# Kernel optimization log

Measured on AMD Instinct MI355X. Metric: run time of the kernel, lower is better.

## Reference

```python
import jax, jax.numpy as jnp
import numpy as np

H = W = 9
C = 16
D = 34
NHEAD = 2
HDIM = D // NHEAD  # 17
FF = 2048
NLAYERS = 2
EPS = 1e-5


def setup_inputs() -> dict:
    key = jax.random.key(0)
    ks = jax.random.split(key, 16)
    s = 0.05
    return {
        "obs": jax.random.normal(ks[0], (2, H, W), dtype=jnp.float32),
        "conv1_w": jax.random.normal(ks[1], (16, 2, 3, 3), dtype=jnp.float32) * s,
        "conv1_b": jnp.zeros((16,), jnp.float32),
        "conv2_w": jax.random.normal(ks[2], (16, 16, 3, 3), dtype=jnp.float32) * s,
        "conv2_b": jnp.zeros((16,), jnp.float32),
        "in_proj_w": jax.random.normal(ks[3], (NLAYERS, 3 * D, D), dtype=jnp.float32) * s,
        "in_proj_b": jnp.zeros((NLAYERS, 3 * D), jnp.float32),
        "out_proj_w": jax.random.normal(ks[4], (NLAYERS, D, D), dtype=jnp.float32) * s,
        "out_proj_b": jnp.zeros((NLAYERS, D), jnp.float32),
        "lin1_w": jax.random.normal(ks[5], (NLAYERS, FF, D), dtype=jnp.float32) * s,
        "lin1_b": jnp.zeros((NLAYERS, FF), jnp.float32),
        "lin2_w": jax.random.normal(ks[6], (NLAYERS, D, FF), dtype=jnp.float32) * s,
        "lin2_b": jnp.zeros((NLAYERS, D), jnp.float32),
        "ln1_g": jnp.ones((NLAYERS, D), jnp.float32),
        "ln1_b": jnp.zeros((NLAYERS, D), jnp.float32),
        "ln2_g": jnp.ones((NLAYERS, D), jnp.float32),
        "ln2_b": jnp.zeros((NLAYERS, D), jnp.float32),
    }


def _layer_norm(x, g, b):
    m = jnp.mean(x, axis=-1, keepdims=True)
    v = jnp.mean(jnp.square(x - m), axis=-1, keepdims=True)
    return (x - m) * jax.lax.rsqrt(v + EPS) * g + b


def _encoder_layer(x, ipw, ipb, opw, opb, l1w, l1b, l2w, l2b, g1, b1, g2, b2):
    # x: [S, D]. Post-norm TransformerEncoderLayer, eval mode (no dropout).
    S = x.shape[0]
    qkv = x @ ipw.T + ipb  # [S, 3D]
    q, k, v = jnp.split(qkv, 3, axis=-1)
    q = q.reshape(S, NHEAD, HDIM).transpose(1, 0, 2)  # [h, S, d]
    k = k.reshape(S, NHEAD, HDIM).transpose(1, 0, 2)
    v = v.reshape(S, NHEAD, HDIM).transpose(1, 0, 2)
    scores = jnp.einsum("hqd,hkd->hqk", q, k) / jnp.sqrt(jnp.float32(HDIM))
    attn = jax.nn.softmax(scores, axis=-1)
    o = jnp.einsum("hqk,hkd->hqd", attn, v)  # [h, S, d]
    o = o.transpose(1, 0, 2).reshape(S, D)
    o = o @ opw.T + opb
    x = _layer_norm(x + o, g1, b1)
    f = jax.nn.relu(x @ l1w.T + l1b) @ l2w.T + l2b
    return _layer_norm(x + f, g2, b2)


def _conv(x, w, b):
    y = jax.lax.conv_general_dilated(
        x, w, window_strides=(1, 1), padding="SAME",
        dimension_numbers=("NCHW", "OIHW", "NCHW"))
    return jax.nn.relu(y + b[None, :, None, None])


def reference(obs, conv1_w, conv1_b, conv2_w, conv2_b, in_proj_w, in_proj_b,
              out_proj_w, out_proj_b, lin1_w, lin1_b, lin2_w, lin2_b,
              ln1_g, ln1_b, ln2_g, ln2_b):
    x = obs[None]  # [1, 2, H, W]
    x = _conv(x, conv1_w, conv1_b)
    x = _conv(x, conv2_w, conv2_b)
    hw = H * W
    cell_emb = x[0].reshape(C, hw).T  # [hw, C]
    idx = jnp.arange(hw)
    r = (idx // W).astype(jnp.float32)
    c = (idx % W).astype(jnp.float32)
    dx = (r[:, None] - r[None, :]) / ((H - 1) / 2.0)  # [hw, hw]
    dy = (c[:, None] - c[None, :]) / ((W - 1) / 2.0)
    tok_i = jnp.broadcast_to(cell_emb[:, None, :], (hw, hw, C))
    tok_j = jnp.broadcast_to(cell_emb[None, :, :], (hw, hw, C))
    rel = jnp.stack([dx, dy], axis=-1)  # [hw, hw, 2]
    tokens = jnp.concatenate([tok_i, tok_j, rel], axis=-1).reshape(hw * hw, D)
    for l in range(NLAYERS):
        tokens = _encoder_layer(
            tokens, in_proj_w[l], in_proj_b[l], out_proj_w[l], out_proj_b[l],
            lin1_w[l], lin1_b[l], lin2_w[l], lin2_b[l],
            ln1_g[l], ln1_b[l], ln2_g[l], ln2_b[l])
    agent_idx = jnp.argmax(obs[0].reshape(-1))
    start = agent_idx * hw
    agent_tokens = jax.lax.dynamic_slice(tokens, (start, 0), (hw, D))
    return agent_tokens.mean(axis=0)  # [D]
```

## Files before the change

### kernel.cpp

```cpp
#include <hip/hip_runtime.h>
#include <hip/hip_bf16.h>

#define HH 9
#define WW 9
#define HW 81
#define CC 16
#define DD 34
#define SS 6561
#define NHEAD 2
#define HD 17
#define FF 2048
#define EPSF 1e-5f

#define NTILES 52
#define NSPLIT2 26
#define QB 64

#define NIP 7168
#define NOP 3072
#define NW1 131072
#define NW2 98304
#define NLTOT (NIP + NOP + NW1 + NW2)
#define LPREP_BLOCKS 1872
#define NKF 425984
#define NVF 212992
#define NV16 13312
#define ZERO_WORDS 332800
#define ZERO_BLOCKS 1300

#define NEAB 124416
#define NVFL1 12288
#define KSPLIT 8

typedef __attribute__((ext_vector_type(8))) short bf16x8;
typedef __attribute__((ext_vector_type(4))) float f32x4;

__device__ __forceinline__ unsigned short f2b(float f) {
  unsigned int u = __float_as_uint(f);
  u += 0x7fffu + ((u >> 16) & 1u);
  return (unsigned short)(u >> 16);
}

__global__ __launch_bounds__(256) void prep_kernel(
    const float* __restrict__ obs, const float* __restrict__ w1, const float* __restrict__ b1,
    const float* __restrict__ w2, const float* __restrict__ b2,
    float* __restrict__ cell, int* __restrict__ aidx,
    const float* __restrict__ ipw, const float* __restrict__ opw,
    const float* __restrict__ l1w, const float* __restrict__ l2w,
    unsigned short* __restrict__ ipwp, unsigned short* __restrict__ opwp,
    unsigned short* __restrict__ w1p, unsigned short* __restrict__ w2p,
    unsigned short* __restrict__ kfp, unsigned short* __restrict__ vfp,
    float* __restrict__ v16) {
  int bx = blockIdx.x;
  int t = threadIdx.x;
  if (bx == 0) {
    __shared__ float s_obs[2][11][11];
    __shared__ float s_w1[288];
    __shared__ float s_w2[2304];
    __shared__ float s_b1[16], s_b2[16];
    __shared__ float y1[CC][121];
    for (int i = t; i < 2 * 121; i += 256) ((float*)s_obs)[i] = 0.f;
    for (int i = t; i < CC * 121; i += 256) ((float*)y1)[i] = 0.f;
    for (int i = t; i < 288; i += 256) s_w1[i] = w1[i];
    for (int i = t; i < 2304; i += 256) s_w2[i] = w2[i];
    if (t < 16) { s_b1[t] = b1[t]; s_b2[t] = b2[t]; }
    __syncthreads();
    for (int i = t; i < 2 * HW; i += 256) {
      int ic = i / HW, p = i % HW;
      s_obs[ic][1 + p / WW][1 + p % WW] = obs[i];
    }
    __syncthreads();
    if (t == 0) {
      int best = 0; float bv = s_obs[0][1][1];
      for (int p = 1; p < HW; p++) {
        float v = s_obs[0][1 + p / WW][1 + p % WW];
        if (v > bv) { bv = v; best = p; }
      }
      *aidx = best;
    }
    for (int idx = t; idx < CC * HW; idx += 256) {
      int c = idx / HW, p = idx % HW;
      int i = p / WW, j = p % WW;
      float acc = s_b1[c];
#pragma unroll
      for (int ic = 0; ic < 2; ic++)
#pragma unroll
        for (int di = 0; di < 3; di++)
#pragma unroll
          for (int dj = 0; dj < 3; dj++)
            acc += s_obs[ic][i + di][j + dj] * s_w1[((c * 2 + ic) * 3 + di) * 3 + dj];
      y1[c][(i + 1) * 11 + (j + 1)] = fmaxf(acc, 0.f);
    }
    __syncthreads();
    for (int idx = t; idx < CC * HW; idx += 256) {
      int c = idx / HW, p = idx % HW;
      int i = p / WW, j = p % WW;
      float acc = s_b2[c];
#pragma unroll
      for (int ic = 0; ic < CC; ic++)
#pragma unroll
        for (int di = 0; di < 3; di++)
#pragma unroll
          for (int dj = 0; dj < 3; dj++)
            acc += y1[ic][(i + di) * 11 + (j + dj)] * s_w2[((c * CC + ic) * 3 + di) * 3 + dj];
      cell[p * CC + c] = fmaxf(acc, 0.f);
    }
  } else if (bx <= LPREP_BLOCKS) {
    int i = (bx - 1) * 256 + t;
    int layer = i / NLTOT;
    int r = i % NLTOT;
    if (r < NIP) {
      int n = r >> 6, k = r & 63;
      ipwp[layer * NIP + r] =
          (n < 102 && k < DD) ? f2b(ipw[(size_t)layer * 102 * DD + n * DD + k]) : (unsigned short)0;
    } else if (r < NIP + NOP) {
      int rr = r - NIP;
      int n = rr >> 6, k = rr & 63;
      opwp[layer * NOP + rr] =
          (n < DD && k < DD) ? f2b(opw[(size_t)layer * DD * DD + n * DD + k]) : (unsigned short)0;
    } else if (r < NIP + NOP + NW1) {
      int rr = r - NIP - NOP;
      int f = rr >> 6, k = rr & 63;
      w1p[layer * NW1 + rr] =
          (k < DD) ? f2b(l1w[(size_t)layer * FF * DD + f * DD + k]) : (unsigned short)0;
    } else {
      int rr = r - NIP - NOP - NW1;
      int d = rr >> 11, kk = rr & 2047;
      w2p[layer * NW2 + rr] =
          (d < DD) ? f2b(l2w[(size_t)layer * DD * FF + d * FF + kk]) : (unsigned short)0;
    }
  } else {
    int zi = (bx - 1 - LPREP_BLOCKS) * 256 + t;
    if (zi < NKF / 2) ((unsigned int*)kfp)[zi] = 0u;
    else if (zi < NKF / 2 + NVF / 2) ((unsigned int*)vfp)[zi - NKF / 2] = 0u;
    else if (zi < ZERO_WORDS) v16[zi - NKF / 2 - NVF / 2] = 0.f;
  }
}

__global__ __launch_bounds__(256) void ptprep_kernel(
    const float* __restrict__ cell, const float* __restrict__ ipw,
    const float* __restrict__ ipb, float* __restrict__ Pt) {
  int idx = blockIdx.x * 256 + threadIdx.x;
  if (idx >= 2 * HW * 102) return;
  int part = idx / (HW * 102);
  int rem = idx % (HW * 102);
  int a = rem / 102, n = rem % 102;
  float ra = (float)(a / WW) * 0.25f, ca = (float)(a % WW) * 0.25f;
  float acc;
  if (part == 0) {
    acc = ipb[n] + ipw[n * DD + 32] * ra + ipw[n * DD + 33] * ca;
    for (int f = 0; f < CC; f++) acc += ipw[n * DD + f] * cell[a * CC + f];
  } else {
    acc = -(ipw[n * DD + 32] * ra + ipw[n * DD + 33] * ca);
    for (int f = 0; f < CC; f++) acc += ipw[n * DD + CC + f] * cell[a * CC + f];
  }
  Pt[idx] = acc;
}

__global__ __launch_bounds__(256) void expprep_kernel(
    const float* __restrict__ Pt, float* __restrict__ eAB,
    unsigned short* __restrict__ vfragL1) {
  int idx = blockIdx.x * 256 + threadIdx.x;
  const float scale = 0.24253562503633297f;
  if (idx < NEAB) {
    int a = idx % 96; int rest = idx / 96;
    int row = rest % 81; rest /= 81;
    int ab = rest & 1, p = (rest >> 1) & 1, h = rest >> 2;
    float e = 0.f;
    if (a < HW) {
      const float* qrow = Pt + (size_t)ab * (HW * 102) + row * 102 + h * HD;
      const float* krow = Pt + (size_t)p * (HW * 102) + a * 102 + DD + h * HD;
      float dot = 0.f;
#pragma unroll
      for (int d = 0; d < HD; d++) dot += qrow[d] * krow[d];
      e = __expf(fminf(dot * scale, 40.f));
    }
    eAB[idx] = e;
  } else if (idx < NEAB + NVFL1) {
    int j = idx - NEAB;
    int a = j % 96; int rest = j / 96;
    int n = rest % 32; rest /= 32;
    int p = rest & 1, h = rest >> 1;
    float v = 0.f;
    if (a < HW) {
      if (n < HD) v = Pt[(size_t)p * (HW * 102) + a * 102 + 2 * DD + h * HD + n];
      else if (n == HD) v = 1.f;
    }
    vfragL1[((size_t)(h * 2 + p) * 32 + n) * 96 + a] = f2b(v);
  }
}

__global__ __launch_bounds__(256) void fl1_kernel(
    const float* __restrict__ cell, const float* __restrict__ eAB,
    const unsigned short* __restrict__ vfragL1,
    const unsigned short* __restrict__ opwp, const float* __restrict__ opb,
    const float* __restrict__ g1v, const float* __restrict__ b1v,
    const unsigned short* __restrict__ w1p, const unsigned short* __restrict__ w2p,
    const float* __restrict__ fb1, const float* __restrict__ fb2,
    const float* __restrict__ g2v, const float* __restrict__ b2v,
    float* __restrict__ x) {
  __shared__ __align__(16) unsigned short sE[4][16 * 96];
  __shared__ __align__(16) unsigned short soA[16 * 72];
  __shared__ float sxF[16][35];
  __shared__ __align__(16) unsigned short sxA2[16 * 72];
  __shared__ float sxF2[16][35];
  __shared__ __align__(16) unsigned short hw_[4][16 * 40];
  __shared__ float yred[4][16][49];
  int t = threadIdx.x;
  int w = t >> 6, lane = t & 63, quad = lane >> 4, col = lane & 15;
  int r0 = blockIdx.x * 16;
  int nr = min(16, SS - r0);

  for (int i = t; i < 16 * 72; i += 256) { soA[i] = 0; sxA2[i] = 0; }
  for (int i = t; i < 16 * 35; i += 256) { ((float*)sxF)[i] = 0.f; ((float*)sxF2)[i] = 0.f; }
  for (int i = t; i < nr * DD; i += 256) {
    int r = i / DD, d = i - r * DD;
    int row = r0 + r;
    int ii = row / HW, jj = row - ii * HW;
    float v;
    if (d < CC) v = cell[ii * CC + d];
    else if (d < 2 * CC) v = cell[jj * CC + (d - CC)];
    else if (d == 32) v = (float)((ii / WW) - (jj / WW)) * 0.25f;
    else v = (float)((ii % WW) - (jj % WW)) * 0.25f;
    sxF[r][d] = v;
  }

  {
    int h = w >> 1, p = w & 1;
    const float* eA = eAB + ((size_t)((h * 2 + p) * 2 + 0) * 81) * 96;
    const float* eB = eAB + ((size_t)((h * 2 + p) * 2 + 1) * 81) * 96;
    int tl = lane >> 2, asub = lane & 3;
    int row = r0 + tl;
    int tc = row < SS ? row : SS - 1;
    int it = tc / HW, jt = tc - it * HW;
    const float* eAr = eA + it * 96 + asub * 24;
    const float* eBr = eB + jt * 96 + asub * 24;
    unsigned short etmp[24];
#pragma unroll
    for (int k = 0; k < 24; k++) etmp[k] = f2b(eAr[k] * eBr[k]);
    unsigned short* Eb = &sE[w][tl * 96 + asub * 24];
#pragma unroll
    for (int k = 0; k < 3; k++)
      *(bf16x8*)(Eb + k * 8) = *(bf16x8*)(etmp + k * 8);
    const unsigned short* vf = vfragL1 + (size_t)(h * 2 + p) * 32 * 96;
    f32x4 acc0 = {0.f, 0.f, 0.f, 0.f}, acc1 = {0.f, 0.f, 0.f, 0.f};
#pragma unroll
    for (int c = 0; c < 3; c++) {
      bf16x8 ea = *(const bf16x8*)&sE[w][col * 96 + c * 32 + quad * 8];
      bf16x8 vb0 = *(const bf16x8*)&vf[col * 96 + c * 32 + quad * 8];
      bf16x8 vb1 = *(const bf16x8*)&vf[(16 + col) * 96 + c * 32 + quad * 8];
      acc0 = __builtin_amdgcn_mfma_f32_16x16x32_bf16(ea, vb0, acc0, 0, 0, 0);
      acc1 = __builtin_amdgcn_mfma_f32_16x16x32_bf16(ea, vb1, acc1, 0, 0, 0);
    }
    float Sr[4];
#pragma unroll
    for (int r = 0; r < 4; r++) Sr[r] = __shfl(acc1[r], (lane & 48) + 1);
#pragma unroll
    for (int r = 0; r < 4; r++) {
      int rr = quad * 4 + r;
      float inv = 1.f / Sr[r];
      yred[w][rr][col] = acc0[r] * inv;
      if (col == 0) yred[w][rr][16] = acc1[r] * inv;
    }
  }
  __syncthreads();
  for (int i = t; i < 16 * DD; i += 256) {
    int r = i / DD, dd = i - r * DD;
    int h2 = dd / HD, d2 = dd - h2 * HD;
    soA[r * 72 + dd] = f2b(yred[2 * h2][r][d2] + yred[2 * h2 + 1][r][d2]);
  }
  __syncthreads();

  if (w == 0) {
    bf16x8 a0 = *(const bf16x8*)&soA[col * 72 + quad * 8];
    bf16x8 a1 = *(const bf16x8*)&soA[col * 72 + 32 + quad * 8];
    f32x4 y[3];
#pragma unroll
    for (int nt = 0; nt < 3; nt++) {
      int n = nt * 16 + col;
      bf16x8 b0 = *(const bf16x8*)&opwp[n * 64 + quad * 8];
      bf16x8 b1 = *(const bf16x8*)&opwp[n * 64 + 32 + quad * 8];
      f32x4 acc = {0.f, 0.f, 0.f, 0.f};
      acc = __builtin_amdgcn_mfma_f32_16x16x32_bf16(a0, b0, acc, 0, 0, 0);
      y[nt] = __builtin_amdgcn_mfma_f32_16x16x32_bf16(a1, b1, acc, 0, 0, 0);
    }
    float yv[3][4];
    float s1[4] = {0.f, 0.f, 0.f, 0.f}, s2[4] = {0.f, 0.f, 0.f, 0.f};
#pragma unroll
    for (int nt = 0; nt < 3; nt++) {
      int d = nt * 16 + col;
      bool vd = d < DD;
      float ob = vd ? opb[d] : 0.f;
#pragma unroll
      for (int r = 0; r < 4; r++) {
        int row = quad * 4 + r;
        float v = vd ? (y[nt][r] + ob + sxF[row][d]) : 0.f;
        yv[nt][r] = v;
        s1[r] += v;
        s2[r] += v * v;
      }
    }
#pragma unroll
    for (int msk = 1; msk <= 8; msk <<= 1)
#pragma unroll
      for (int r = 0; r < 4; r++) {
        s1[r] += __shfl_xor(s1[r], msk);
        s2[r] += __shfl_xor(s2[r], msk);
      }
#pragma unroll
    for (int r = 0; r < 4; r++) {
      int row = quad * 4 + r;
      float mean = s1[r] * (1.f / DD);
      float var = s2[r] * (1.f / DD) - mean * mean;
      float rs = rsqrtf(var + EPSF);
#pragma unroll
      for (int nt = 0; nt < 3; nt++) {
        int d = nt * 16 + col;
        if (d < DD) {
          float o = (yv[nt][r] - mean) * rs * g1v[d] + b1v[d];
          sxF2[row][d] = o;
          sxA2[row * 72 + d] = f2b(o);
        }
      }
    }
  }
  __syncthreads();

  bf16x8 a0 = *(const bf16x8*)&sxA2[col * 72 + quad * 8];
  bf16x8 a1 = *(const bf16x8*)&sxA2[col * 72 + 32 + quad * 8];
  unsigned short* myh = &hw_[w][0];
  f32x4 acc3[3];
#pragma unroll
  for (int nt = 0; nt < 3; nt++) acc3[nt] = (f32x4){0.f, 0.f, 0.f, 0.f};
  for (int kt = 0; kt < 16; kt++) {
    int fbase = kt * 128 + w * 32;
#pragma unroll
    for (int nt = 0; nt < 2; nt++) {
      int f = fbase + nt * 16 + col;
      bf16x8 b0f = *(const bf16x8*)&w1p[f * 64 + quad * 8];
      bf16x8 b1f = *(const bf16x8*)&w1p[f * 64 + 32 + quad * 8];
      f32x4 hacc = {0.f, 0.f, 0.f, 0.f};
      hacc = __builtin_amdgcn_mfma_f32_16x16x32_bf16(a0, b0f, hacc, 0, 0, 0);
      hacc = __builtin_amdgcn_mfma_f32_16x16x32_bf16(a1, b1f, hacc, 0, 0, 0);
      float bias = fb1[f];
#pragma unroll
      for (int r = 0; r < 4; r++) {
        float hv = fmaxf(hacc[r] + bias, 0.f);
        myh[(quad * 4 + r) * 40 + nt * 16 + col] = f2b(hv);
      }
    }
    bf16x8 pa = *(const bf16x8*)&myh[col * 40 + quad * 8];
#pragma unroll
    for (int nt = 0; nt < 3; nt++) {
      int n = nt * 16 + col;
      bf16x8 wb = *(const bf16x8*)&w2p[(size_t)n * FF + fbase + quad * 8];
      acc3[nt] = __builtin_amdgcn_mfma_f32_16x16x32_bf16(pa, wb, acc3[nt], 0, 0, 0);
    }
  }
#pragma unroll
  for (int nt = 0; nt < 3; nt++)
#pragma unroll
    for (int r = 0; r < 4; r++)
      yred[w][quad * 4 + r][nt * 16 + col] = acc3[nt][r];
  __syncthreads();
  if (w == 0) {
    float yv[3][4];
    float s1[4] = {0.f, 0.f, 0.f, 0.f}, s2[4] = {0.f, 0.f, 0.f, 0.f};
#pragma unroll
    for (int nt = 0; nt < 3; nt++) {
      int d = nt * 16 + col;
      bool valid = d < DD;
      float b2x = valid ? fb2[d] : 0.f;
#pragma unroll
      for (int r = 0; r < 4; r++) {
        int row = quad * 4 + r;
        float v = yred[0][row][nt * 16 + col] + yred[1][row][nt * 16 + col]
                + yred[2][row][nt * 16 + col] + yred[3][row][nt * 16 + col];
        v = valid ? (v + b2x + sxF2[row][d]) : 0.f;
        yv[nt][r] = v;
        s1[r] += v;
        s2[r] += v * v;
      }
    }
#pragma unroll
    for (int msk = 1; msk <= 8; msk <<= 1)
#pragma unroll
      for (int r = 0; r < 4; r++) {
        s1[r] += __shfl_xor(s1[r], msk);
        s2[r] += __shfl_xor(s2[r], msk);
      }
#pragma unroll
    for (int r = 0; r < 4; r++) {
      int row = quad * 4 + r;
      if (row >= nr) continue;
      float mean = s1[r] * (1.f / DD);
      float var = s2[r] * (1.f / DD) - mean * mean;
      float rs = rsqrtf(var + EPSF);
#pragma unroll
      for (int nt = 0; nt < 3; nt++) {
        int d = nt * 16 + col;
        if (d < DD)
          x[(size_t)(r0 + row) * DD + d] = (yv[nt][r] - mean) * rs * g2v[d] + b2v[d];
      }
    }
  }
}

__global__ __launch_bounds__(256) void qkv2_kernel(
    const float* __restrict__ x, const unsigned short* __restrict__ ipwp,
    const float* __restrict__ ipb, const int* __restrict__ abase,
    float* __restrict__ qkv, unsigned short* __restrict__ kfp,
    unsigned short* __restrict__ vfp, float* __restrict__ v16) {
  __shared__ __align__(16) unsigned short sxA[32 * 72];
  int t = threadIdx.x;
  int w = t >> 6, lane = t & 63, quad = lane >> 4, col = lane & 15;
  int m0 = (w & 1) * 16, half = w >> 1;
  bool qpart = blockIdx.x >= 206;
  int row0 = qpart ? (abase[0] * HW + (blockIdx.x - 206) * 32) : blockIdx.x * 32;
  int nr = min(32, SS - row0);
  for (int i = t; i < 32 * 72; i += 256) sxA[i] = 0;
  __syncthreads();
  for (int i = t; i < nr * DD; i += 256) {
    int r = i / DD, d = i - r * DD;
    sxA[r * 72 + d] = f2b(x[(size_t)(row0 + r) * DD + d]);
  }
  __syncthreads();
  bf16x8 a0 = *(const bf16x8*)&sxA[(m0 + col) * 72 + quad * 8];
  bf16x8 a1 = *(const bf16x8*)&sxA[(m0 + col) * 72 + 32 + quad * 8];
  if (!qpart) {
    int ntc = half ? 2 : 3;
    for (int nt2 = 0; nt2 < ntc; nt2++) {
      int nt = half * 3 + nt2;
      int n = DD + nt * 16 + col;
      int nc = n < 112 ? n : 111;
      bf16x8 b0 = *(const bf16x8*)&ipwp[nc * 64 + quad * 8];
      bf16x8 b1 = *(const bf16x8*)&ipwp[nc * 64 + 32 + quad * 8];
      f32x4 acc = {0.f, 0.f, 0.f, 0.f};
      acc = __builtin_amdgcn_mfma_f32_16x16x32_bf16(a0, b0, acc, 0, 0, 0);
      acc = __builtin_amdgcn_mfma_f32_16x16x32_bf16(a1, b1, acc, 0, 0, 0);
      if (n < 102) {
        float bias = ipb[n];
        int kd = n - DD;
#pragma unroll
        for (int r = 0; r < 4; r++) {
          int m = m0 + quad * 4 + r;
          if (m >= nr) continue;
          int tok = row0 + m;
          float val = acc[r] + bias;
          int T = tok >> 7, tl = tok & 127;
          if (kd < 2 * HD) {
            int h = kd >= HD;
            int d = kd - h * HD;
            int colf = tl >> 3, ntk = tl & 7;
            kfp[(((size_t)h * NTILES + T) * 8 + ntk) * 512 +
                ((d >> 3) * 16 + colf) * 8 + (d & 7)] = f2b(val);
          } else {
            int vd = kd - 2 * HD;
            int h = vd >= HD;
            int d = vd - h * HD;
            if (d < 16) {
              int c = tl >> 5, qf = (tl >> 3) & 3, j = tl & 7;
              vfp[(((size_t)h * NTILES + T) * 4 + c) * 512 +
                  (qf * 16 + d) * 8 + j] = f2b(val);
            } else {
              v16[(size_t)h * (NTILES * 128) + tok] = val;
            }
          }
        }
      }
    }
  } else {
    int ntc = half ? 1 : 2;
    for (int nt2 = 0; nt2 < ntc; nt2++) {
      int nt = half * 2 + nt2;
      int n = nt * 16 + col;
      bf16x8 b0 = *(const bf16x8*)&ipwp[n * 64 + quad * 8];
      bf16x8 b1 = *(const bf16x8*)&ipwp[n * 64 + 32 + quad * 8];
      f32x4 acc = {0.f, 0.f, 0.f, 0.f};
      acc = __builtin_amdgcn_mfma_f32_16x16x32_bf16(a0, b0, acc, 0, 0, 0);
      acc = __builtin_amdgcn_mfma_f32_16x16x32_bf16(a1, b1, acc, 0, 0, 0);
      if (n < DD) {
        float bias = ipb[n];
#pragma unroll
        for (int r = 0; r < 4; r++) {
          int m = row0 + m0 + quad * 4 + r;
          if (m < SS) qkv[(size_t)m * 102 + n] = acc[r] + bias;
        }
      }
    }
  }
}

__global__ __launch_bounds__(256) void attn2_kernel(
    const float* __restrict__ qkv, const unsigned short* __restrict__ kfp,
    const unsigned short* __restrict__ vfp, const float* __restrict__ v16,
    const int* __restrict__ abase,
    float* __restrict__ opart, float* __restrict__ lpart) {
  __shared__ __align__(16) unsigned short scb[4][16 * 136];
  int t = threadIdx.x, w = t >> 6, lane = t & 63, quad = lane >> 4, col = lane & 15;
  int h = blockIdx.y, sp = blockIdx.z;
  int base = abase[0] * HW;
  int q0 = blockIdx.x * QB;
  const float scale = 0.24253562503633297f;
  const unsigned short* kf = kfp + (size_t)h * (NTILES * 8 * 512);
  const unsigned short* vf = vfp + (size_t)h * (NTILES * 4 * 512);
  const float* v16h = v16 + (size_t)h * (NTILES * 128);
  unsigned short* myscb = &scb[w][0];

  int mq = base + q0 + w * 16 + col;
  int qc = mq < SS ? mq : SS - 1;
  bf16x8 aq;
#pragma unroll
  for (int j = 0; j < 8; j++) {
    int d = quad * 8 + j;
    aq[j] = (short)((d < HD) ? f2b(qkv[(size_t)qc * 102 + h * HD + d] * scale) : 0);
  }

  f32x4 oacc = {0.f, 0.f, 0.f, 0.f};
  float o16a[4] = {0.f, 0.f, 0.f, 0.f};
  float lreg[4] = {0.f, 0.f, 0.f, 0.f};

  for (int tile = sp; tile < NTILES; tile += NSPLIT2) {
    int k0 = tile * 128;
    const unsigned short* kt = kf + (size_t)tile * (8 * 512);
    f32x4 s[8];
#pragma unroll
    for (int nt = 0; nt < 8; nt++) {
      bf16x8 kb = *(const bf16x8*)(kt + nt * 512 + lane * 8);
      f32x4 z = {0.f, 0.f, 0.f, 0.f};
      s[nt] = __builtin_amdgcn_mfma_f32_16x16x32_bf16(aq, kb, z, 0, 0, 0);
    }
    if (k0 + 128 > SS) {
#pragma unroll
      for (int nt = 0; nt < 8; nt++)
        if (k0 + col * 8 + nt >= SS) {
          s[nt][0] = -1e30f; s[nt][1] = -1e30f; s[nt][2] = -1e30f; s[nt][3] = -1e30f;
        }
    }
#pragma unroll
    for (int r = 0; r < 4; r++) {
      bf16x8 pv;
      float psl = 0.f;
#pragma unroll
      for (int nt = 0; nt < 8; nt++) {
        float p = __expf(fminf(s[nt][r], 70.f));
        s[nt][r] = p;
        psl += p;
        pv[nt] = (short)f2b(p);
      }
      lreg[r] += psl;
      *(bf16x8*)(myscb + (quad * 4 + r) * 136 + col * 8) = pv;
    }
    f32x4 va = *(const f32x4*)(v16h + k0 + col * 8);
    f32x4 vb4 = *(const f32x4*)(v16h + k0 + col * 8 + 4);
#pragma unroll
    for (int r = 0; r < 4; r++) {
      o16a[r] += s[0][r] * va[0] + s[1][r] * va[1] + s[2][r] * va[2] + s[3][r] * va[3]
               + s[4][r] * vb4[0] + s[5][r] * vb4[1] + s[6][r] * vb4[2] + s[7][r] * vb4[3];
    }
    const unsigned short* vt = vf + (size_t)tile * (4 * 512);
#pragma unroll
    for (int c = 0; c < 4; c++) {
      bf16x8 pa = *(const bf16x8*)(myscb + col * 136 + c * 32 + quad * 8);
      bf16x8 vbf = *(const bf16x8*)(vt + c * 512 + lane * 8);
      oacc = __builtin_amdgcn_mfma_f32_16x16x32_bf16(pa, vbf, oacc, 0, 0, 0);
    }
  }
#pragma unroll
  for (int msk = 1; msk <= 8; msk <<= 1)
#pragma unroll
    for (int r = 0; r < 4; r++) {
      o16a[r] += __shfl_xor(o16a[r], msk);
      lreg[r] += __shfl_xor(lreg[r], msk);
    }
  size_t obase = ((size_t)sp * NHEAD + h) * 128;
#pragma unroll
  for (int r = 0; r < 4; r++) {
    int ql = q0 + w * 16 + quad * 4 + r;
    if (ql < HW) {
      opart[(obase + ql) * HD + col] = oacc[r];
      if (col == 0) {
        opart[(obase + ql) * HD + 16] = o16a[r];
        lpart[obase + ql] = lreg[r];
      }
    }
  }
}

__global__ __launch_bounds__(256) void fl2a_kernel(
    const float* __restrict__ opart, const float* __restrict__ lpart,
    const unsigned short* __restrict__ opwp, const float* __restrict__ opb,
    const float* __restrict__ g1v, const float* __restrict__ b1v,
    const unsigned short* __restrict__ w1p, const unsigned short* __restrict__ w2p,
    const float* __restrict__ fb1, const int* __restrict__ abase,
    const float* __restrict__ x, float* __restrict__ xln, float* __restrict__ ypart) {
  __shared__ __align__(16) unsigned short soA[16 * 72];
  __shared__ float sxF[16][35];
  __shared__ __align__(16) unsigned short sxA2[16 * 72];
  __shared__ float sxF2[16][35];
  __shared__ __align__(16) unsigned short hw_[4][16 * 40];
  __shared__ float yred[4][16][49];
  int t = threadIdx.x;
  int w = t >> 6, lane = t & 63, quad = lane >> 4, col = lane & 15;
  int sp = blockIdx.y;
  int base = abase[0] * HW;
  int ql0 = blockIdx.x * 16;
  int nr = min(16, HW - ql0);
  int r0 = base + ql0;

  for (int i = t; i < 16 * 72; i += 256) { soA[i] = 0; sxA2[i] = 0; }
  for (int i = t; i < 16 * 35; i += 256) { ((float*)sxF)[i] = 0.f; ((float*)sxF2)[i] = 0.f; }
  __syncthreads();
  for (int i = t; i < nr * DD; i += 256) {
    int r = i / DD, rem = i - r * DD;
    sxF[r][rem] = x[(size_t)(r0 + r) * DD + rem];
    int ql = ql0 + r;
    int h = rem / HD, d = rem - h * HD;
    float L = 0.f, O = 0.f;
#pragma unroll
    for (int s = 0; s < NSPLIT2; s++) {
      L += lpart[((size_t)s * NHEAD + h) * 128 + ql];
      O += opart[(((size_t)s * NHEAD + h) * 128 + ql) * HD + d];
    }
    soA[r * 72 + rem] = f2b(O / L);
  }
  __syncthreads();
  if (w == 0) {
    bf16x8 a0 = *(const bf16x8*)&soA[col * 72 + quad * 8];
    bf16x8 a1 = *(const bf16x8*)&soA[col * 72 + 32 + quad * 8];
    f32x4 y[3];
#pragma unroll
    for (int nt = 0; nt < 3; nt++) {
      int n = nt * 16 + col;
      bf16x8 b0 = *(const bf16x8*)&opwp[n * 64 + quad * 8];
      bf16x8 b1 = *(const bf16x8*)&opwp[n * 64 + 32 + quad * 8];
      f32x4 acc = {0.f, 0.f, 0.f, 0.f};
      acc = __builtin_amdgcn_mfma_f32_16x16x32_bf16(a0, b0, acc, 0, 0, 0);
      y[nt] = __builtin_amdgcn_mfma_f32_16x16x32_bf16(a1, b1, acc, 0, 0, 0);
    }
    float yv[3][4];
    float s1[4] = {0.f, 0.f, 0.f, 0.f}, s2[4] = {0.f, 0.f, 0.f, 0.f};
#pragma unroll
    for (int nt = 0; nt < 3; nt++) {
      int d = nt * 16 + col;
      bool vd = d < DD;
      float ob = vd ? opb[d] : 0.f;
#pragma unroll
      for (int r = 0; r < 4; r++) {
        int row = quad * 4 + r;
        float v = vd ? (y[nt][r] + ob + sxF[row][d]) : 0.f;
        yv[nt][r] = v;
        s1[r] += v;
        s2[r] += v * v;
      }
    }
#pragma unroll
    for (int msk = 1; msk <= 8; msk <<= 1)
#pragma unroll
      for (int r = 0; r < 4; r++) {
        s1[r] += __shfl_xor(s1[r], msk);
        s2[r] += __shfl_xor(s2[r], msk);
      }
#pragma unroll
    for (int r = 0; r < 4; r++) {
      int row = quad * 4 + r;
      float mean = s1[r] * (1.f / DD);
      float var = s2[r] * (1.f / DD) - mean * mean;
      float rs = rsqrtf(var + EPSF);
#pragma unroll
      for (int nt = 0; nt < 3; nt++) {
        int d = nt * 16 + col;
        if (d < DD) {
          float o = (yv[nt][r] - mean) * rs * g1v[d] + b1v[d];
          sxF2[row][d] = o;
          sxA2[row * 72 + d] = f2b(o);
          if (sp == 0 && row < nr)
            xln[(size_t)(ql0 + row) * DD + d] = o;
        }
      }
    }
  }
  __syncthreads();
  bf16x8 a0 = *(const bf16x8*)&sxA2[col * 72 + quad * 8];
  bf16x8 a1 = *(const bf16x8*)&sxA2[col * 72 + 32 + quad * 8];
  unsigned short* myh = &hw_[w][0];
  f32x4 acc3[3];
#pragma unroll
  for (int nt = 0; nt < 3; nt++) acc3[nt] = (f32x4){0.f, 0.f, 0.f, 0.f};
  for (int kt2 = 0; kt2 < 2; kt2++) {
    int kt = sp * 2 + kt2;
    int fbase = kt * 128 + w * 32;
#pragma unroll
    for (int nt = 0; nt < 2; nt++) {
      int f = fbase + nt * 16 + col;
      bf16x8 b0f = *(const bf16x8*)&w1p[f * 64 + quad * 8];
      bf16x8 b1f = *(const bf16x8*)&w1p[f * 64 + 32 + quad * 8];
      f32x4 hacc = {0.f, 0.f, 0.f, 0.f};
      hacc = __builtin_amdgcn_mfma_f32_16x16x32_bf16(a0, b0f, hacc, 0, 0, 0);
      hacc = __builtin_amdgcn_mfma_f32_16x16x32_bf16(a1, b1f, hacc, 0, 0, 0);
      float bias = fb1[f];
#pragma unroll
      for (int r = 0; r < 4; r++) {
        float hv = fmaxf(hacc[r] + bias, 0.f);
        myh[(quad * 4 + r) * 40 + nt * 16 + col] = f2b(hv);
      }
    }
    bf16x8 pa = *(const bf16x8*)&myh[col * 40 + quad * 8];
#pragma unroll
    for (int nt = 0; nt < 3; nt++) {
      int n = nt * 16 + col;
      bf16x8 wb = *(const bf16x8*)&w2p[(size_t)n * FF + fbase + quad * 8];
      acc3[nt] = __builtin_amdgcn_mfma_f32_16x16x32_bf16(pa, wb, acc3[nt], 0, 0, 0);
    }
  }
#pragma unroll
  for (int nt = 0; nt < 3; nt++)
#pragma unroll
    for (int r = 0; r < 4; r++)
      yred[w][quad * 4 + r][nt * 16 + col] = acc3[nt][r];
  __syncthreads();
  if (w == 0) {
    for (int i = lane; i < nr * DD; i += 64) {
      int r = i / DD, d = i - r * DD;
      float v = yred[0][r][d] + yred[1][r][d] + yred[2][r][d] + yred[3][r][d];
      ypart[((size_t)sp * HW + ql0 + r) * DD + d] = v;
    }
  }
}

__global__ __launch_bounds__(256) void fl2b_kernel(
    const float* __restrict__ ypart, const float* __restrict__ xln,
    const float* __restrict__ fb2, const float* __restrict__ g2v,
    const float* __restrict__ b2v, const int* __restrict__ abase,
    float* __restrict__ x) {
  int t = threadIdx.x;
  int row = blockIdx.x * 32 + (t >> 3);
  int s8 = t & 7;
  if (row >= HW) return;
  int base = abase[0] * HW;
  float yv[5];
  float s1 = 0.f, s2 = 0.f;
  int cnt = 0;
  for (int d = s8; d < DD; d += 8) {
    float v = fb2[d] + xln[(size_t)row * DD + d];
#pragma unroll
    for (int sp = 0; sp < KSPLIT; sp++)
      v += ypart[((size_t)sp * HW + row) * DD + d];
    yv[cnt++] = v;
    s1 += v;
    s2 += v * v;
  }
  s1 += __shfl_xor(s1, 1); s2 += __shfl_xor(s2, 1);
  s1 += __shfl_xor(s1, 2); s2 += __shfl_xor(s2, 2);
  s1 += __shfl_xor(s1, 4); s2 += __shfl_xor(s2, 4);
  float mean = s1 * (1.f / DD);
  float var = s2 * (1.f / DD) - mean * mean;
  float rs = rsqrtf(var + EPSF);
  cnt = 0;
  for (int d = s8; d < DD; d += 8)
    x[(size_t)(base + row) * DD + d] = (yv[cnt++] - mean) * rs * g2v[d] + b2v[d];
}

__global__ __launch_bounds__(64) void final_kernel(
    const float* __restrict__ x, const int* __restrict__ aidx, float* __restrict__ out) {
  int d = threadIdx.x;
  if (d >= DD) return;
  int start = (*aidx) * HW;
  float acc = 0.f;
  for (int j = 0; j < HW; j++) acc += x[(size_t)(start + j) * DD + d];
  out[d] = acc * (1.f / HW);
}

extern "C" void kernel_launch(void* const* d_in, const int* in_sizes, int n_in,
                              void* d_out, int out_size, void* d_ws, size_t ws_size,
                              hipStream_t stream) {
  const float* obs = (const float*)d_in[0];
  const float* c1w = (const float*)d_in[1];
  const float* c1b = (const float*)d_in[2];
  const float* c2w = (const float*)d_in[3];
  const float* c2b = (const float*)d_in[4];
  const float* ipw = (const float*)d_in[5];
  const float* ipb = (const float*)d_in[6];
  const float* opw = (const float*)d_in[7];
  const float* opb = (const float*)d_in[8];
  const float* l1w = (const float*)d_in[9];
  const float* l1b = (const float*)d_in[10];
  const float* l2w = (const float*)d_in[11];
  const float* l2b = (const float*)d_in[12];
  const float* g1 = (const float*)d_in[13];
  const float* b1 = (const float*)d_in[14];
  const float* g2 = (const float*)d_in[15];
  const float* b2 = (const float*)d_in[16];
  float* out = (float*)d_out;

  float* ws = (float*)d_ws;
  size_t off = 0;
  float* x     = ws + off; off += SS * DD;
  float* qkv   = ws + off; off += SS * 102;
  float* cell  = ws + off; off += HW * CC;
  int*   aidx  = (int*)(ws + off); off += 1;
  off = (off + 3) & ~(size_t)3;
  float* Pt    = ws + off; off += 2 * HW * 102;
  float* opart = ws + off; off += (size_t)NSPLIT2 * NHEAD * 128 * HD;
  float* lpart = ws + off; off += (size_t)NSPLIT2 * NHEAD * 128;
  float* eAB   = ws + off; off += NEAB;
  float* xln   = ws + off; off += HW * DD;
  float* ypart = ws + off; off += (size_t)KSPLIT * HW * DD;
  off = (off + 3) & ~(size_t)3;
  unsigned short* vfragL1 = (unsigned short*)(ws + off); off += NVFL1 / 2;
  unsigned short* kfp  = (unsigned short*)(ws + off); off += NKF / 2;
  unsigned short* vfp  = (unsigned short*)(ws + off); off += NVF / 2;
  float* v16 = ws + off; off += NV16;
  unsigned short* ipwp = (unsigned short*)(ws + off); off += 2 * NIP / 2;
  unsigned short* opwp = (unsigned short*)(ws + off); off += 2 * NOP / 2;
  unsigned short* w1p  = (unsigned short*)(ws + off); off += 2 * NW1 / 2;
  unsigned short* w2p  = (unsigned short*)(ws + off); off += 2 * NW2 / 2;

  const int prep_grid = 1 + LPREP_BLOCKS + ZERO_BLOCKS;
  const int pt_blocks = (2 * HW * 102 + 255) / 256;
  const int exp_blocks = (NEAB + NVFL1 + 255) / 256;
  const int fl1_blocks = (SS + 15) / 16;

  prep_kernel<<<prep_grid, 256, 0, stream>>>(
      obs, c1w, c1b, c2w, c2b, cell, aidx,
      ipw, opw, l1w, l2w, ipwp, opwp, w1p, w2p, kfp, vfp, v16);
  ptprep_kernel<<<pt_blocks, 256, 0, stream>>>(cell, ipw, ipb, Pt);
  expprep_kernel<<<exp_blocks, 256, 0, stream>>>(Pt, eAB, vfragL1);
  fl1_kernel<<<fl1_blocks, 256, 0, stream>>>(
      cell, eAB, vfragL1, opwp, opb, g1, b1, w1p, w2p, l1b, l2b, g2, b2, x);
  qkv2_kernel<<<210, 256, 0, stream>>>(
      x, ipwp + NIP, ipb + 102, aidx, qkv, kfp, vfp, v16);
  dim3 a2g(2, NHEAD, NSPLIT2);
  attn2_kernel<<<a2g, 256, 0, stream>>>(qkv, kfp, vfp, v16, aidx, opart, lpart);
  dim3 f2g(6, KSPLIT);
  fl2a_kernel<<<f2g, 256, 0, stream>>>(
      opart, lpart, opwp + NOP, opb + DD, g1 + DD, b1 + DD,
      w1p + NW1, w2p + NW2, l1b + FF, aidx, x, xln, ypart);
  fl2b_kernel<<<3, 256, 0, stream>>>(
      ypart, xln, l2b + DD, g2 + DD, b2 + DD, aidx, x);
  final_kernel<<<1, 64, 0, stream>>>(x, aidx, out);
}
```

Baseline: 187.5 us.

## Split layer-1 FFN over the hidden dim and add a reduction kernel

The fused layer-1 kernel now runs two blocks per 16-row tile, each covering half of the 2048-wide FFN hidden dimension. Each block writes a partial FFN output plus the post-attention layernorm result to workspace, and a new reduction kernel sums the partials and applies the bias, residual and second layernorm. qkv2 also moves from 32-row to 16-row tiles, doubling its grid. The intent is more parallelism and shorter per-block FFN loops, at the cost of recomputing attention per split, an extra launch, and extra global traffic for the partials.

```diff
diff --git a/kernel.cpp b/kernel.cpp
--- a/kernel.cpp
+++ b/kernel.cpp
@@ -31,6 +31,7 @@
 #define NEAB 124416
 #define NVFL1 12288
 #define KSPLIT 8
+#define KS1 2
 
 typedef __attribute__((ext_vector_type(8))) short bf16x8;
 typedef __attribute__((ext_vector_type(4))) float f32x4;
@@ -190,29 +191,28 @@
   }
 }
 
-__global__ __launch_bounds__(256) void fl1_kernel(
+__global__ __launch_bounds__(256) void fl1a_kernel(
     const float* __restrict__ cell, const float* __restrict__ eAB,
     const unsigned short* __restrict__ vfragL1,
     const unsigned short* __restrict__ opwp, const float* __restrict__ opb,
     const float* __restrict__ g1v, const float* __restrict__ b1v,
     const unsigned short* __restrict__ w1p, const unsigned short* __restrict__ w2p,
-    const float* __restrict__ fb1, const float* __restrict__ fb2,
-    const float* __restrict__ g2v, const float* __restrict__ b2v,
-    float* __restrict__ x) {
+    const float* __restrict__ fb1,
+    float* __restrict__ xlnL1, float* __restrict__ ypart1) {
   __shared__ __align__(16) unsigned short sE[4][16 * 96];
   __shared__ __align__(16) unsigned short soA[16 * 72];
   __shared__ float sxF[16][35];
   __shared__ __align__(16) unsigned short sxA2[16 * 72];
-  __shared__ float sxF2[16][35];
   __shared__ __align__(16) unsigned short hw_[4][16 * 40];
   __shared__ float yred[4][16][49];
   int t = threadIdx.x;
   int w = t >> 6, lane = t & 63, quad = lane >> 4, col = lane & 15;
+  int sp = blockIdx.y;
   int r0 = blockIdx.x * 16;
   int nr = min(16, SS - r0);
 
   for (int i = t; i < 16 * 72; i += 256) { soA[i] = 0; sxA2[i] = 0; }
-  for (int i = t; i < 16 * 35; i += 256) { ((float*)sxF)[i] = 0.f; ((float*)sxF2)[i] = 0.f; }
+  for (int i = t; i < 16 * 35; i += 256) ((float*)sxF)[i] = 0.f;
   for (int i = t; i < nr * DD; i += 256) {
     int r = i / DD, d = i - r * DD;
     int row = r0 + r;
@@ -318,8 +318,9 @@
         int d = nt * 16 + col;
         if (d < DD) {
           float o = (yv[nt][r] - mean) * rs * g1v[d] + b1v[d];
-          sxF2[row][d] = o;
           sxA2[row * 72 + d] = f2b(o);
+          if (sp == 0 && row < nr)
+            xlnL1[(size_t)(r0 + row) * DD + d] = o;
         }
       }
     }
@@ -332,7 +333,8 @@
   f32x4 acc3[3];
 #pragma unroll
   for (int nt = 0; nt < 3; nt++) acc3[nt] = (f32x4){0.f, 0.f, 0.f, 0.f};
-  for (int kt = 0; kt < 16; kt++) {
+  for (int kt2 = 0; kt2 < 8; kt2++) {
+    int kt = sp * 8 + kt2;
     int fbase = kt * 128 + w * 32;
 #pragma unroll
     for (int nt = 0; nt < 2; nt++) {
@@ -364,46 +366,43 @@
       yred[w][quad * 4 + r][nt * 16 + col] = acc3[nt][r];
   __syncthreads();
   if (w == 0) {
-    float yv[3][4];
-    float s1[4] = {0.f, 0.f, 0.f, 0.f}, s2[4] = {0.f, 0.f, 0.f, 0.f};
-#pragma unroll
-    for (int nt = 0; nt < 3; nt++) {
-      int d = nt * 16 + col;
-      bool valid = d < DD;
-      float b2x = valid ? fb2[d] : 0.f;
-#pragma unroll
-      for (int r = 0; r < 4; r++) {
-        int row = quad * 4 + r;
-        float v = yred[0][row][nt * 16 + col] + yred[1][row][nt * 16 + col]
-                + yred[2][row][nt * 16 + col] + yred[3][row][nt * 16 + col];
-        v = valid ? (v + b2x + sxF2[row][d]) : 0.f;
-        yv[nt][r] = v;
-        s1[r] += v;
-        s2[r] += v * v;
-      }
-    }
-#pragma unroll
-    for (int msk = 1; msk <= 8; msk <<= 1)
-#pragma unroll
-      for (int r = 0; r < 4; r++) {
-        s1[r] += __shfl_xor(s1[r], msk);
-        s2[r] += __shfl_xor(s2[r], msk);
-      }
-#pragma unroll
-    for (int r = 0; r < 4; r++) {
-      int row = quad * 4 + r;
-      if (row >= nr) continue;
-      float mean = s1[r] * (1.f / DD);
-      float var = s2[r] * (1.f / DD) - mean * mean;
-      float rs = rsqrtf(var + EPSF);
-#pragma unroll
-      for (int nt = 0; nt < 3; nt++) {
-        int d = nt * 16 + col;
-        if (d < DD)
-          x[(size_t)(r0 + row) * DD + d] = (yv[nt][r] - mean) * rs * g2v[d] + b2v[d];
-      }
-    }
-  }
+    for (int i = lane; i < nr * DD; i += 64) {
+      int r = i / DD, d = i - r * DD;
+      float v = yred[0][r][d] + yred[1][r][d] + yred[2][r][d] + yred[3][r][d];
+      ypart1[((size_t)sp * SS + r0 + r) * DD + d] = v;
+    }
+  }
+}
+
+__global__ __launch_bounds__(256) void fl1b_kernel(
+    const float* __restrict__ ypart1, const float* __restrict__ xlnL1,
+    const float* __restrict__ fb2, const float* __restrict__ g2v,
+    const float* __restrict__ b2v, float* __restrict__ x) {
+  int t = threadIdx.x;
+  int row = blockIdx.x * 32 + (t >> 3);
+  int s8 = t & 7;
+  if (row >= SS) return;
+  float yv[5];
+  float s1 = 0.f, s2 = 0.f;
+  int cnt = 0;
+  for (int d = s8; d < DD; d += 8) {
+    float v = fb2[d] + xlnL1[(size_t)row * DD + d];
+#pragma unroll
+    for (int sp = 0; sp < KS1; sp++)
+      v += ypart1[((size_t)sp * SS + row) * DD + d];
+    yv[cnt++] = v;
+    s1 += v;
+    s2 += v * v;
+  }
+  s1 += __shfl_xor(s1, 1); s2 += __shfl_xor(s2, 1);
+  s1 += __shfl_xor(s1, 2); s2 += __shfl_xor(s2, 2);
+  s1 += __shfl_xor(s1, 4); s2 += __shfl_xor(s2, 4);
+  float mean = s1 * (1.f / DD);
+  float var = s2 * (1.f / DD) - mean * mean;
+  float rs = rsqrtf(var + EPSF);
+  cnt = 0;
+  for (int d = s8; d < DD; d += 8)
+    x[(size_t)row * DD + d] = (yv[cnt++] - mean) * rs * g2v[d] + b2v[d];
 }
 
 __global__ __launch_bounds__(256) void qkv2_kernel(
@@ -411,26 +410,25 @@
     const float* __restrict__ ipb, const int* __restrict__ abase,
     float* __restrict__ qkv, unsigned short* __restrict__ kfp,
     unsigned short* __restrict__ vfp, float* __restrict__ v16) {
-  __shared__ __align__(16) unsigned short sxA[32 * 72];
+  __shared__ __align__(16) unsigned short sxA[16 * 72];
   int t = threadIdx.x;
   int w = t >> 6, lane = t & 63, quad = lane >> 4, col = lane & 15;
-  int m0 = (w & 1) * 16, half = w >> 1;
-  bool qpart = blockIdx.x >= 206;
-  int row0 = qpart ? (abase[0] * HW + (blockIdx.x - 206) * 32) : blockIdx.x * 32;
-  int nr = min(32, SS - row0);
-  for (int i = t; i < 32 * 72; i += 256) sxA[i] = 0;
+  bool qpart = blockIdx.x >= 411;
+  int row0 = qpart ? (abase[0] * HW + (blockIdx.x - 411) * 16) : blockIdx.x * 16;
+  int nr = min(16, SS - row0);
+  for (int i = t; i < 16 * 72; i += 256) sxA[i] = 0;
   __syncthreads();
   for (int i = t; i < nr * DD; i += 256) {
     int r = i / DD, d = i - r * DD;
     sxA[r * 72 + d] = f2b(x[(size_t)(row0 + r) * DD + d]);
   }
   __syncthreads();
-  bf16x8 a0 = *(const bf16x8*)&sxA[(m0 + col) * 72 + quad * 8];
-  bf16x8 a1 = *(const bf16x8*)&sxA[(m0 + col) * 72 + 32 + quad * 8];
+  bf16x8 a0 = *(const bf16x8*)&sxA[col * 72 + quad * 8];
+  bf16x8 a1 = *(const bf16x8*)&sxA[col * 72 + 32 + quad * 8];
   if (!qpart) {
-    int ntc = half ? 2 : 3;
-    for (int nt2 = 0; nt2 < ntc; nt2++) {
-      int nt = half * 3 + nt2;
+    int npass = (w == 0) ? 2 : 1;
+    for (int pass = 0; pass < npass; pass++) {
+      int nt = (pass == 0) ? w : 4;
       int n = DD + nt * 16 + col;
       int nc = n < 112 ? n : 111;
       bf16x8 b0 = *(const bf16x8*)&ipwp[nc * 64 + quad * 8];
@@ -443,7 +441,7 @@
         int kd = n - DD;
 #pragma unroll
         for (int r = 0; r < 4; r++) {
-          int m = m0 + quad * 4 + r;
+          int m = quad * 4 + r;
           if (m >= nr) continue;
           int tok = row0 + m;
           float val = acc[r] + bias;
@@ -470,10 +468,8 @@
       }
     }
   } else {
-    int ntc = half ? 1 : 2;
-    for (int nt2 = 0; nt2 < ntc; nt2++) {
-      int nt = half * 2 + nt2;
-      int n = nt * 16 + col;
+    if (w < 3) {
+      int n = w * 16 + col;
       bf16x8 b0 = *(const bf16x8*)&ipwp[n * 64 + quad * 8];
       bf16x8 b1 = *(const bf16x8*)&ipwp[n * 64 + 32 + quad * 8];
       f32x4 acc = {0.f, 0.f, 0.f, 0.f};
@@ -483,7 +479,7 @@
         float bias = ipb[n];
 #pragma unroll
         for (int r = 0; r < 4; r++) {
-          int m = row0 + m0 + quad * 4 + r;
+          int m = row0 + quad * 4 + r;
           if (m < SS) qkv[(size_t)m * 102 + n] = acc[r] + bias;
         }
       }
@@ -597,7 +593,6 @@
   __shared__ __align__(16) unsigned short soA[16 * 72];
   __shared__ float sxF[16][35];
   __shared__ __align__(16) unsigned short sxA2[16 * 72];
-  __shared__ float sxF2[16][35];
   __shared__ __align__(16) unsigned short hw_[4][16 * 40];
   __shared__ float yred[4][16][49];
   int t = threadIdx.x;
@@ -609,7 +604,7 @@
   int r0 = base + ql0;
 
   for (int i = t; i < 16 * 72; i += 256) { soA[i] = 0; sxA2[i] = 0; }
-  for (int i = t; i < 16 * 35; i += 256) { ((float*)sxF)[i] = 0.f; ((float*)sxF2)[i] = 0.f; }
+  for (int i = t; i < 16 * 35; i += 256) ((float*)sxF)[i] = 0.f;
   __syncthreads();
   for (int i = t; i < nr * DD; i += 256) {
     int r = i / DD, rem = i - r * DD;
@@ -672,7 +667,6 @@
         int d = nt * 16 + col;
         if (d < DD) {
           float o = (yv[nt][r] - mean) * rs * g1v[d] + b1v[d];
-          sxF2[row][d] = o;
           sxA2[row * 72 + d] = f2b(o);
           if (sp == 0 && row < nr)
             xln[(size_t)(ql0 + row) * DD + d] = o;
@@ -804,6 +798,8 @@
   float* opart = ws + off; off += (size_t)NSPLIT2 * NHEAD * 128 * HD;
   float* lpart = ws + off; off += (size_t)NSPLIT2 * NHEAD * 128;
   float* eAB   = ws + off; off += NEAB;
+  float* xlnL1 = ws + off; off += SS * DD;
+  float* ypart1 = ws + off; off += (size_t)KS1 * SS * DD;
   float* xln   = ws + off; off += HW * DD;
   float* ypart = ws + off; off += (size_t)KSPLIT * HW * DD;
   off = (off + 3) & ~(size_t)3;
@@ -820,15 +816,19 @@
   const int pt_blocks = (2 * HW * 102 + 255) / 256;
   const int exp_blocks = (NEAB + NVFL1 + 255) / 256;
   const int fl1_blocks = (SS + 15) / 16;
+  const int red_blocks = (SS + 31) / 32;
 
   prep_kernel<<<prep_grid, 256, 0, stream>>>(
       obs, c1w, c1b, c2w, c2b, cell, aidx,
       ipw, opw, l1w, l2w, ipwp, opwp, w1p, w2p, kfp, vfp, v16);
   ptprep_kernel<<<pt_blocks, 256, 0, stream>>>(cell, ipw, ipb, Pt);
   expprep_kernel<<<exp_blocks, 256, 0, stream>>>(Pt, eAB, vfragL1);
-  fl1_kernel<<<fl1_blocks, 256, 0, stream>>>(
-      cell, eAB, vfragL1, opwp, opb, g1, b1, w1p, w2p, l1b, l2b, g2, b2, x);
-  qkv2_kernel<<<210, 256, 0, stream>>>(
+  dim3 f1g(fl1_blocks, KS1);
+  fl1a_kernel<<<f1g, 256, 0, stream>>>(
+      cell, eAB, vfragL1, opwp, opb, g1, b1, w1p, w2p, l1b, xlnL1, ypart1);
+  fl1b_kernel<<<red_blocks, 256, 0, stream>>>(
+      ypart1, xlnL1, l2b, g2, b2, x);
+  qkv2_kernel<<<419, 256, 0, stream>>>(
       x, ipwp + NIP, ipb + 102, aidx, qkv, kfp, vfp, v16);
   dim3 a2g(2, NHEAD, NSPLIT2);
   attn2_kernel<<<a2g, 256, 0, stream>>>(qkv, kfp, vfp, v16, aidx, opart, lpart);
```

Result: no change. 189.3 us (+1.0%).
